# Optimization experiments

Hardware: AMD Instinct MI355X
Metric: run time of the kernel (lower is better)

Reference implementation:

```python
import jax, jax.numpy as jnp
import numpy as np

B, N, C, E, M = 16, 4096, 128, 12288, 64  # batch, nodes(seq_len), channels, incidences, hyperedges
NEG_SLOPE = 0.2
MARGIN = 4.2


def setup_inputs() -> dict:
    key = jax.random.key(0)
    k1, k2, k3, k4, k5 = jax.random.split(key, 5)
    x = jax.random.normal(k1, (B, N, C), jnp.float32)
    hyperedge_nodes = jax.random.randint(k2, (E,), 0, N)
    hyperedge_edges = jax.random.randint(k3, (E,), 0, M)
    weight = jax.random.normal(k4, (C, C), jnp.float32) * (1.0 / np.sqrt(C))  # glorot-ish
    att = jax.random.normal(k5, (1, 1, 2 * C), jnp.float32) * 0.1  # heads=1
    return {"x": x, "hyperedge_nodes": hyperedge_nodes, "hyperedge_edges": hyperedge_edges,
            "weight": weight, "att": att}


def _segment_softmax(logits, seg, num_segments):
    # logits: [E, B], softmax within groups of seg (per node)
    smax = jax.ops.segment_max(logits, seg, num_segments=num_segments)
    e = jnp.exp(logits - smax[seg])
    ssum = jax.ops.segment_sum(e, seg, num_segments=num_segments)
    return e / (ssum[seg] + 1e-16)


def reference(x, hyperedge_nodes, hyperedge_edges, weight, att):
    nodes = hyperedge_nodes
    edges = hyperedge_edges
    xw = jnp.matmul(x, weight)            # [B, N, C]
    x1 = jnp.swapaxes(xw, 0, 1)           # [N, B, C]

    x_gath = x1[nodes]                    # [E, B, C] gather by node id
    x_i = x_gath
    # per-hyperedge sum of incident node features (the python dict loop in torch)
    edge_sums = jax.ops.segment_sum(x_gath, edges, num_segments=M)  # [M, B, C]
    x_j = edge_sums[edges]                # [E, B, C]

    # O(M^2) pairwise hyperedge loss (vectorized)
    sq = jnp.sum(edge_sums * edge_sums, axis=-1)          # [M, B]
    norms = jnp.sqrt(sq)                                   # [M, B]
    inner = jnp.einsum('mbc,nbc->mnb', edge_sums, edge_sums)  # [M, M, B]
    cos = inner / (norms[:, None, :] * norms[None, :, :])      # [M, M, B]
    dist = jnp.sqrt(jnp.clip(sq[:, None, :] + sq[None, :, :] - 2.0 * inner, 0.0))
    loss_item = cos * dist + (1.0 - cos) * jnp.maximum(MARGIN - dist, 0.0)  # [M, M, B]
    loss_hyper = jnp.sum(jnp.abs(jnp.mean(loss_item, axis=-1))) / float((M + 1) ** 2)

    # attention per incidence, softmax grouped by node
    alpha = jnp.sum(jnp.concatenate([x_i, x_j], axis=-1) * att, axis=-1)  # [E, B]
    alpha = jax.nn.leaky_relu(alpha, NEG_SLOPE)
    alpha = _segment_softmax(alpha, nodes, N)  # [E, B] (dropout: eval mode, identity)

    ones = jnp.ones((E,), x.dtype)
    D = jax.ops.segment_sum(ones, nodes, num_segments=N)   # node degree
    Bdeg = jax.ops.segment_sum(ones, edges, num_segments=M)
    Bn = jnp.where(Bdeg > 0, 1.0 / Bdeg, 0.0)              # 1/deg, inf -> 0

    # propagate source_to_target: nodes -> hyperedges
    msg1 = Bn[edges][:, None, None] * x1[nodes] * alpha[:, :, None]   # [E, B, C]
    out_e = jax.ops.segment_sum(msg1, edges, num_segments=M)          # [M, B, C]
    # propagate target_to_source: hyperedges -> nodes
    msg2 = D[nodes][:, None, None] * out_e[edges] * alpha[:, :, None]
    out = jax.ops.segment_sum(msg2, nodes, num_segments=N)            # [N, B, C]
    out = jnp.swapaxes(out, 0, 1)                                     # [B, N, C]

    constrain_total = jnp.abs(jnp.mean(x_i - x_j)) + loss_hyper
    return (out, constrain_total)
```

## Files before the change

### kernel.cpp

```cpp
#include <hip/hip_runtime.h>
#include <hip/hip_bf16.h>

#define Bc 16
#define Nn 4096
#define Cc 128
#define Ee 12288
#define Mm 64
#define NEG_SLOPE 0.2f
#define MARGIN 4.2f
#define CH 4

__global__ __launch_bounds__(256) void gemm_xw(const float* __restrict__ x,
                                               const float* __restrict__ w,
                                               const float* __restrict__ att,
                                               float* __restrict__ xw,
                                               float* __restrict__ p,
                                               float* __restrict__ S1) {
    __shared__ float xT[64][132];
    __shared__ float wl[64][132];
    int t = threadIdx.x;
    int tc = t & 15;
    int tr = t >> 4;
    int rowbase = blockIdx.x * 128;

    float acc[8][8];
#pragma unroll
    for (int i = 0; i < 8; i++)
#pragma unroll
        for (int j = 0; j < 8; j++) acc[i][j] = 0.f;

    for (int half = 0; half < 2; ++half) {
#pragma unroll
        for (int s = 0; s < 8; ++s) {
            int idx = s * 256 + t;
            int row = idx >> 4, k4 = idx & 15;
            float4 v = ((const float4*)x)[(size_t)(rowbase + row) * 32 + half * 16 + k4];
            xT[k4 * 4 + 0][row] = v.x;
            xT[k4 * 4 + 1][row] = v.y;
            xT[k4 * 4 + 2][row] = v.z;
            xT[k4 * 4 + 3][row] = v.w;
        }
#pragma unroll
        for (int s = 0; s < 8; ++s) {
            int idx = s * 256 + t;
            int k = idx >> 5, c4 = idx & 31;
            float4 v = ((const float4*)w)[(size_t)(half * 64 + k) * 32 + c4];
            *(float4*)&wl[k][c4 * 4] = v;
        }
        __syncthreads();
#pragma unroll 4
        for (int k = 0; k < 64; ++k) {
            float4 xv0 = *(const float4*)&xT[k][tr * 8];
            float4 xv1 = *(const float4*)&xT[k][tr * 8 + 4];
            float4 wv0 = *(const float4*)&wl[k][tc * 8];
            float4 wv1 = *(const float4*)&wl[k][tc * 8 + 4];
            float xs_[8] = {xv0.x, xv0.y, xv0.z, xv0.w, xv1.x, xv1.y, xv1.z, xv1.w};
            float ww_[8] = {wv0.x, wv0.y, wv0.z, wv0.w, wv1.x, wv1.y, wv1.z, wv1.w};
#pragma unroll
            for (int i = 0; i < 8; i++)
#pragma unroll
                for (int j = 0; j < 8; j++) acc[i][j] += xs_[i] * ww_[j];
        }
        __syncthreads();
    }

    float4 a0 = ((const float4*)att)[tc * 2];
    float4 a1 = ((const float4*)att)[tc * 2 + 1];
    float aw[8] = {a0.x, a0.y, a0.z, a0.w, a1.x, a1.y, a1.z, a1.w};
#pragma unroll
    for (int i = 0; i < 8; i++) {
        int rr = rowbase + tr * 8 + i;
        int b = rr >> 12;
        int n = rr & 4095;
        ((float4*)xw)[(size_t)n * 512 + b * 32 + tc * 2] =
            make_float4(acc[i][0], acc[i][1], acc[i][2], acc[i][3]);
        ((float4*)xw)[(size_t)n * 512 + b * 32 + tc * 2 + 1] =
            make_float4(acc[i][4], acc[i][5], acc[i][6], acc[i][7]);
        float pd = 0.f, ss = 0.f;
#pragma unroll
        for (int j = 0; j < 8; j++) { pd += acc[i][j] * aw[j]; ss += acc[i][j]; }
#pragma unroll
        for (int m = 1; m < 16; m <<= 1) {
            pd += __shfl_xor(pd, m, 64);
            ss += __shfl_xor(ss, m, 64);
        }
        if (tc == 0) {
            p[n * 16 + b] = pd;
            atomicAdd(&S1[n], ss);
        }
    }
}

__global__ void hist_kernel(const int* __restrict__ nodes, const int* __restrict__ edges,
                            int* __restrict__ deg_n, int* __restrict__ deg_m) {
    int e = blockIdx.x * 256 + threadIdx.x;
    if (e < Ee) {
        atomicAdd(&deg_n[nodes[e]], 1);
        atomicAdd(&deg_m[edges[e]], 1);
    }
}

__global__ __launch_bounds__(1024) void scan_kernel(const int* __restrict__ deg_n,
                                                    const int* __restrict__ deg_m,
                                                    int* __restrict__ off_n, int* __restrict__ off_m,
                                                    int* __restrict__ cur_n, int* __restrict__ cur_m) {
    __shared__ int s[1024];
    int t = threadIdx.x;
    int base = t * 4;
    int d0 = deg_n[base], d1 = deg_n[base + 1], d2 = deg_n[base + 2], d3 = deg_n[base + 3];
    int local = d0 + d1 + d2 + d3;
    s[t] = local;
    __syncthreads();
    for (int offs = 1; offs < 1024; offs <<= 1) {
        int v = (t >= offs) ? s[t - offs] : 0;
        __syncthreads();
        s[t] += v;
        __syncthreads();
    }
    int excl = s[t] - local;
    int o0 = excl, o1 = excl + d0, o2 = excl + d0 + d1, o3 = excl + d0 + d1 + d2;
    off_n[base] = o0; off_n[base + 1] = o1; off_n[base + 2] = o2; off_n[base + 3] = o3;
    cur_n[base] = o0; cur_n[base + 1] = o1; cur_n[base + 2] = o2; cur_n[base + 3] = o3;
    if (t == 1023) off_n[4096] = s[1023];
    if (t == 0) {
        int acc = 0;
        for (int m = 0; m < 64; m++) {
            off_m[m] = acc; cur_m[m] = acc; acc += deg_m[m];
        }
        off_m[64] = acc;
    }
}

__global__ void fill_kernel(const int* __restrict__ nodes, const int* __restrict__ edges,
                            int* __restrict__ cur_n, int* __restrict__ cur_m,
                            int* __restrict__ list_n, int* __restrict__ gedge_n,
                            int* __restrict__ list_m, int* __restrict__ gnode_m) {
    int e = blockIdx.x * 256 + threadIdx.x;
    if (e < Ee) {
        int n = nodes[e], m = edges[e];
        int pos = atomicAdd(&cur_n[n], 1);
        list_n[pos] = e;
        gedge_n[pos] = m;
        int pos2 = atomicAdd(&cur_m[m], 1);
        list_m[pos2] = e;
        gnode_m[pos2] = n;
    }
}

__global__ __launch_bounds__(256) void edge_sums_kernel(const float* __restrict__ xw,
                                                        const int* __restrict__ off_m,
                                                        const int* __restrict__ gnode_m,
                                                        float* __restrict__ es) {
    int m = blockIdx.x;
    int slot = blockIdx.y * 256 + threadIdx.x;
    int beg = off_m[m], end = off_m[m + 1];
    int len = end - beg;
    int cbeg = beg + (len * (int)blockIdx.z) / CH;
    int cend = beg + (len * ((int)blockIdx.z + 1)) / CH;
    float acc = 0.f;
    for (int i = cbeg; i < cend; i++) {
        int n = gnode_m[i];
        acc += xw[(size_t)n * 2048 + slot];
    }
    if (acc != 0.f || cend > cbeg) atomicAdd(&es[m * 2048 + slot], acc);
}

__global__ __launch_bounds__(256) void edge_stats_kernel(const float* __restrict__ es,
                                                         const float* __restrict__ att,
                                                         float* __restrict__ q,
                                                         float* __restrict__ sq,
                                                         float* __restrict__ T) {
    int m = blockIdx.x, t = threadIdx.x;
    int b = t >> 4, oc = (t & 15) * 8;
    const float* row = es + m * 2048 + b * 128 + oc;
    float qd = 0.f, sqd = 0.f, s = 0.f;
#pragma unroll
    for (int j = 0; j < 8; j++) {
        float v = row[j];
        qd += v * att[128 + oc + j];
        sqd += v * v;
        s += v;
    }
    for (int k = 1; k < 16; k <<= 1) {
        qd += __shfl_xor(qd, k, 64);
        sqd += __shfl_xor(sqd, k, 64);
        s += __shfl_xor(s, k, 64);
    }
    if ((t & 15) == 0) { q[m * 16 + b] = qd; sq[m * 16 + b] = sqd; }
    s += __shfl_xor(s, 16, 64);
    s += __shfl_xor(s, 32, 64);
    __shared__ float ws4[4];
    if ((t & 63) == 0) ws4[t >> 6] = s;
    __syncthreads();
    if (t == 0) T[m] = ws4[0] + ws4[1] + ws4[2] + ws4[3];
}

__global__ __launch_bounds__(256) void loss_kernel(const float* __restrict__ es,
                                                   const float* __restrict__ sq,
                                                   float* __restrict__ loss_part) {
    int m = blockIdx.x, t = threadIdx.x;
    __shared__ float esm[2048];
    for (int i = t; i < 2048; i += 256) esm[i] = es[m * 2048 + i];
    __syncthreads();
    int n = t >> 2, bq = t & 3;
    float part = 0.f;
#pragma unroll
    for (int u = 0; u < 4; u++) {
        int b = bq * 4 + u;
        float inner = 0.f;
        const float* er = es + n * 2048 + b * 128;
        const float* em = esm + b * 128;
        for (int c = 0; c < 128; c += 4) {
            float4 a = *(const float4*)(em + c);
            float4 o = *(const float4*)(er + c);
            inner += a.x * o.x + a.y * o.y + a.z * o.z + a.w * o.w;
        }
        float sm = sq[m * 16 + b], sn = sq[n * 16 + b];
        float cosv = inner / (sqrtf(sm) * sqrtf(sn));
        float d2 = sm + sn - 2.f * inner;
        float dist = sqrtf(fmaxf(d2, 0.f));
        part += cosv * dist + (1.f - cosv) * fmaxf(MARGIN - dist, 0.f);
    }
    part += __shfl_xor(part, 1, 64);
    part += __shfl_xor(part, 2, 64);
    float labs = fabsf(part * (1.f / 16.f));
    __shared__ float pl[64];
    if (bq == 0) pl[n] = labs;
    __syncthreads();
    if (t < 64) {
        float v = pl[t];
        for (int k = 1; k < 64; k <<= 1) v += __shfl_xor(v, k, 64);
        if (t == 0) loss_part[m] = v;
    }
}

__global__ __launch_bounds__(256) void alpha_kernel(const int* __restrict__ off_n,
                                                    const int* __restrict__ list_n,
                                                    const int* __restrict__ gedge_n,
                                                    const float* __restrict__ p,
                                                    const float* __restrict__ q,
                                                    float* __restrict__ alpha) {
    int idx = blockIdx.x * 256 + threadIdx.x;
    int b = idx & 15, n = idx >> 4;
    int beg = off_n[n], end = off_n[n + 1];
    if (beg == end) return;
    float pb = p[n * 16 + b];
    float lf = pb + q[gedge_n[beg] * 16 + b];
    lf = lf >= 0.f ? lf : NEG_SLOPE * lf;
    float ssum = 0.f;
    for (int i = beg; i < end; i++) {
        float l = pb + q[gedge_n[i] * 16 + b];
        l = l >= 0.f ? l : NEG_SLOPE * l;
        ssum += __expf(l - lf);
    }
    float inv = 1.f / ssum;
    for (int i = beg; i < end; i++) {
        int e = list_n[i];
        float l = pb + q[gedge_n[i] * 16 + b];
        l = l >= 0.f ? l : NEG_SLOPE * l;
        alpha[e * 16 + b] = __expf(l - lf) * inv;
    }
}

__global__ __launch_bounds__(256) void out_e_kernel(const float* __restrict__ xw,
                                                    const int* __restrict__ off_m,
                                                    const int* __restrict__ list_m,
                                                    const int* __restrict__ gnode_m,
                                                    const float* __restrict__ alpha,
                                                    float* __restrict__ oute) {
    int m = blockIdx.x;
    int slot = blockIdx.y * 256 + threadIdx.x;
    int b = slot >> 7;
    int beg = off_m[m], end = off_m[m + 1];
    int len = end - beg;
    int cbeg = beg + (len * (int)blockIdx.z) / CH;
    int cend = beg + (len * ((int)blockIdx.z + 1)) / CH;
    float acc = 0.f;
    for (int i = cbeg; i < cend; i++) {
        int n = gnode_m[i];
        int e = list_m[i];
        acc += alpha[e * 16 + b] * xw[(size_t)n * 2048 + slot];
    }
    if (cend > cbeg) atomicAdd(&oute[m * 2048 + slot], acc);
}

__global__ __launch_bounds__(256) void out_kernel(const float* __restrict__ oute,
                                                  const int* __restrict__ off_n,
                                                  const int* __restrict__ list_n,
                                                  const int* __restrict__ gedge_n,
                                                  const int* __restrict__ deg_m,
                                                  const float* __restrict__ alpha,
                                                  float* __restrict__ out) {
    int n = blockIdx.x, t = threadIdx.x;
    int beg = off_n[n], end = off_n[n + 1];
    float d = (float)(end - beg);
    float acc[8] = {0, 0, 0, 0, 0, 0, 0, 0};
    for (int i = beg; i < end; i++) {
        int e = list_n[i];
        int m = gedge_n[i];
        float bn = 1.f / (float)deg_m[m];
        const float* er = oute + m * 2048;
#pragma unroll
        for (int k = 0; k < 8; k++) {
            int slot = t + k * 256;
            int b = slot >> 7;
            acc[k] += alpha[e * 16 + b] * bn * er[slot];
        }
    }
#pragma unroll
    for (int k = 0; k < 8; k++) {
        int slot = t + k * 256;
        int b = slot >> 7, c = slot & 127;
        out[(size_t)b * 524288 + n * 128 + c] = d * acc[k];
    }
}

__global__ __launch_bounds__(256) void finalize_kernel(const int* __restrict__ deg_n,
                                                       const float* __restrict__ S1,
                                                       const int* __restrict__ deg_m,
                                                       const float* __restrict__ T,
                                                       const float* __restrict__ loss_part,
                                                       float* __restrict__ out_scalar) {
    int t = threadIdx.x;
    double a = 0.0;
    for (int n = t; n < 4096; n += 256) a += (double)deg_n[n] * (double)S1[n];
    double bsum = 0.0, l = 0.0;
    if (t < 64) {
        bsum = (double)deg_m[t] * (double)T[t];
        l = (double)loss_part[t];
    }
    __shared__ double sa[256], sb[256], sl[256];
    sa[t] = a; sb[t] = bsum; sl[t] = l;
    __syncthreads();
    for (int s = 128; s > 0; s >>= 1) {
        if (t < s) { sa[t] += sa[t + s]; sb[t] += sb[t + s]; sl[t] += sl[t + s]; }
        __syncthreads();
    }
    if (t == 0) {
        double mean = (sa[0] - sb[0]) / 25165824.0;
        out_scalar[0] = (float)(fabs(mean) + sl[0] / 4225.0);
    }
}

extern "C" void kernel_launch(void* const* d_in, const int* in_sizes, int n_in,
                              void* d_out, int out_size, void* d_ws, size_t ws_size,
                              hipStream_t stream) {
    const float* x = (const float*)d_in[0];
    const int* nodes = (const int*)d_in[1];
    const int* edges = (const int*)d_in[2];
    const float* w = (const float*)d_in[3];
    const float* att = (const float*)d_in[4];
    float* out = (float*)d_out;

    char* ws = (char*)d_ws;
    size_t o = 0;
    float* xw = (float*)(ws + o);        o += (size_t)Nn * Bc * Cc * 4;
    size_t zbase = o;
    float* es = (float*)(ws + o);        o += (size_t)Mm * Bc * Cc * 4;
    float* oute = (float*)(ws + o);      o += (size_t)Mm * Bc * Cc * 4;
    int* deg_n = (int*)(ws + o);         o += (size_t)Nn * 4;
    int* deg_m = (int*)(ws + o);         o += (size_t)Mm * 4;
    float* S1 = (float*)(ws + o);        o += (size_t)Nn * 4;
    size_t zlen = o - zbase;
    float* p = (float*)(ws + o);         o += (size_t)Nn * Bc * 4;
    float* q = (float*)(ws + o);         o += (size_t)Mm * Bc * 4;
    float* sq = (float*)(ws + o);        o += (size_t)Mm * Bc * 4;
    float* alpha = (float*)(ws + o);     o += (size_t)Ee * Bc * 4;
    float* T = (float*)(ws + o);         o += (size_t)Mm * 4;
    float* loss_part = (float*)(ws + o); o += (size_t)Mm * 4;
    int* off_n = (int*)(ws + o);         o += (size_t)(Nn + 1) * 4;
    int* off_m = (int*)(ws + o);         o += (size_t)(Mm + 1) * 4;
    int* cur_n = (int*)(ws + o);         o += (size_t)Nn * 4;
    int* cur_m = (int*)(ws + o);         o += (size_t)Mm * 4;
    int* list_n = (int*)(ws + o);        o += (size_t)Ee * 4;
    int* gedge_n = (int*)(ws + o);       o += (size_t)Ee * 4;
    int* list_m = (int*)(ws + o);        o += (size_t)Ee * 4;
    int* gnode_m = (int*)(ws + o);       o += (size_t)Ee * 4;

    hipMemsetAsync(ws + zbase, 0, zlen, stream);

    gemm_xw<<<512, 256, 0, stream>>>(x, w, att, xw, p, S1);
    hist_kernel<<<48, 256, 0, stream>>>(nodes, edges, deg_n, deg_m);
    scan_kernel<<<1, 1024, 0, stream>>>(deg_n, deg_m, off_n, off_m, cur_n, cur_m);
    fill_kernel<<<48, 256, 0, stream>>>(nodes, edges, cur_n, cur_m,
                                        list_n, gedge_n, list_m, gnode_m);
    edge_sums_kernel<<<dim3(Mm, 8, CH), 256, 0, stream>>>(xw, off_m, gnode_m, es);
    edge_stats_kernel<<<Mm, 256, 0, stream>>>(es, att, q, sq, T);
    loss_kernel<<<Mm, 256, 0, stream>>>(es, sq, loss_part);
    alpha_kernel<<<256, 256, 0, stream>>>(off_n, list_n, gedge_n, p, q, alpha);
    out_e_kernel<<<dim3(Mm, 8, CH), 256, 0, stream>>>(xw, off_m, list_m, gnode_m, alpha, oute);
    out_kernel<<<Nn, 256, 0, stream>>>(oute, off_n, list_n, gedge_n, deg_m, alpha, out);
    finalize_kernel<<<1, 256, 0, stream>>>(deg_n, S1, deg_m, T, loss_part, out + (size_t)Bc * Nn * Cc);
}
```

Baseline: 257.5 us.

## Compute XW GEMM with split-bf16 MFMA instead of FP32 FMA

Replaces the FP32 SIMT tiled GEMM with bf16 MFMA instructions. Weight and x are each split into high and low bf16 parts, and three MFMAs (hi*hi, hi*lo, lo*hi) approximate FP32 precision. A small pre-kernel splits and swizzles the weight into LDS-friendly layout, and the GEMM loads the whole weight into LDS once per block. This aims to cut the cost of the 65536x128x128 GEMM, at the price of an extra kernel launch, slightly lower precision than true FP32, and scalar (non-vectorized) xw stores.

```diff
diff --git a/kernel.cpp b/kernel.cpp
--- a/kernel.cpp
+++ b/kernel.cpp
@@ -10,83 +10,122 @@
 #define MARGIN 4.2f
 #define CH 4
 
+typedef __attribute__((ext_vector_type(8))) short bfrag;
+typedef __attribute__((ext_vector_type(4))) float f32x4;
+
+__device__ inline unsigned short f2bf_rne(float f) {
+    unsigned u = __float_as_uint(f);
+    unsigned r = u + 0x7FFFu + ((u >> 16) & 1u);
+    return (unsigned short)(r >> 16);
+}
+__device__ inline float bfbits2f(unsigned short h) {
+    return __uint_as_float(((unsigned)h) << 16);
+}
+
+__global__ __launch_bounds__(256) void wsplit_kernel(const float* __restrict__ w,
+                                                     unsigned short* __restrict__ wsplit) {
+    int idx = blockIdx.x * 256 + threadIdx.x;
+    int k = idx >> 7, c = idx & 127;
+    float v = w[k * 128 + c];
+    unsigned short h = f2bf_rne(v);
+    float r = v - bfbits2f(h);
+    unsigned short lo = f2bf_rne(r);
+    int byteoff = c * 256 + ((2 * k) ^ ((c & 7) << 4));
+    *(unsigned short*)((char*)wsplit + byteoff) = h;
+    *(unsigned short*)((char*)wsplit + 32768 + byteoff) = lo;
+}
+
 __global__ __launch_bounds__(256) void gemm_xw(const float* __restrict__ x,
-                                               const float* __restrict__ w,
+                                               const unsigned short* __restrict__ wsplit,
                                                const float* __restrict__ att,
                                                float* __restrict__ xw,
                                                float* __restrict__ p,
                                                float* __restrict__ S1) {
-    __shared__ float xT[64][132];
-    __shared__ float wl[64][132];
+    __shared__ unsigned short wlds[32768];
     int t = threadIdx.x;
-    int tc = t & 15;
-    int tr = t >> 4;
-    int rowbase = blockIdx.x * 128;
-
-    float acc[8][8];
-#pragma unroll
-    for (int i = 0; i < 8; i++)
-#pragma unroll
-        for (int j = 0; j < 8; j++) acc[i][j] = 0.f;
-
-    for (int half = 0; half < 2; ++half) {
-#pragma unroll
-        for (int s = 0; s < 8; ++s) {
-            int idx = s * 256 + t;
-            int row = idx >> 4, k4 = idx & 15;
-            float4 v = ((const float4*)x)[(size_t)(rowbase + row) * 32 + half * 16 + k4];
-            xT[k4 * 4 + 0][row] = v.x;
-            xT[k4 * 4 + 1][row] = v.y;
-            xT[k4 * 4 + 2][row] = v.z;
-            xT[k4 * 4 + 3][row] = v.w;
-        }
-#pragma unroll
-        for (int s = 0; s < 8; ++s) {
-            int idx = s * 256 + t;
-            int k = idx >> 5, c4 = idx & 31;
-            float4 v = ((const float4*)w)[(size_t)(half * 64 + k) * 32 + c4];
-            *(float4*)&wl[k][c4 * 4] = v;
-        }
-        __syncthreads();
-#pragma unroll 4
-        for (int k = 0; k < 64; ++k) {
-            float4 xv0 = *(const float4*)&xT[k][tr * 8];
-            float4 xv1 = *(const float4*)&xT[k][tr * 8 + 4];
-            float4 wv0 = *(const float4*)&wl[k][tc * 8];
-            float4 wv1 = *(const float4*)&wl[k][tc * 8 + 4];
-            float xs_[8] = {xv0.x, xv0.y, xv0.z, xv0.w, xv1.x, xv1.y, xv1.z, xv1.w};
-            float ww_[8] = {wv0.x, wv0.y, wv0.z, wv0.w, wv1.x, wv1.y, wv1.z, wv1.w};
-#pragma unroll
-            for (int i = 0; i < 8; i++)
-#pragma unroll
-                for (int j = 0; j < 8; j++) acc[i][j] += xs_[i] * ww_[j];
-        }
-        __syncthreads();
-    }
-
-    float4 a0 = ((const float4*)att)[tc * 2];
-    float4 a1 = ((const float4*)att)[tc * 2 + 1];
-    float aw[8] = {a0.x, a0.y, a0.z, a0.w, a1.x, a1.y, a1.z, a1.w};
-#pragma unroll
-    for (int i = 0; i < 8; i++) {
-        int rr = rowbase + tr * 8 + i;
-        int b = rr >> 12;
-        int n = rr & 4095;
-        ((float4*)xw)[(size_t)n * 512 + b * 32 + tc * 2] =
-            make_float4(acc[i][0], acc[i][1], acc[i][2], acc[i][3]);
-        ((float4*)xw)[(size_t)n * 512 + b * 32 + tc * 2 + 1] =
-            make_float4(acc[i][4], acc[i][5], acc[i][6], acc[i][7]);
-        float pd = 0.f, ss = 0.f;
-#pragma unroll
-        for (int j = 0; j < 8; j++) { pd += acc[i][j] * aw[j]; ss += acc[i][j]; }
-#pragma unroll
-        for (int m = 1; m < 16; m <<= 1) {
-            pd += __shfl_xor(pd, m, 64);
-            ss += __shfl_xor(ss, m, 64);
-        }
-        if (tc == 0) {
-            p[n * 16 + b] = pd;
-            atomicAdd(&S1[n], ss);
+    {
+        const float4* g4 = (const float4*)wsplit;
+        float4* l4 = (float4*)wlds;
+#pragma unroll
+        for (int i = 0; i < 16; ++i) l4[i * 256 + t] = g4[i * 256 + t];
+    }
+    __syncthreads();
+
+    int w = t >> 6;
+    int l = t & 63;
+    int lrow = l & 15;
+    int lk = l >> 4;
+    int rowbase = blockIdx.x * 128 + w * 32;
+
+    f32x4 acc[2][8];
+#pragma unroll
+    for (int ti = 0; ti < 2; ++ti)
+#pragma unroll
+        for (int tj = 0; tj < 8; ++tj) acc[ti][tj] = (f32x4){0.f, 0.f, 0.f, 0.f};
+
+    for (int ks = 0; ks < 4; ++ks) {
+        bfrag bh[8], bl[8];
+        int kbyte = (64 * ks + 16 * lk) ^ ((l & 7) << 4);
+#pragma unroll
+        for (int tj = 0; tj < 8; ++tj) {
+            const char* base = (const char*)wlds + (tj * 16 + lrow) * 256 + kbyte;
+            bh[tj] = *(const bfrag*)base;
+            bl[tj] = *(const bfrag*)(base + 32768);
+        }
+#pragma unroll
+        for (int ti = 0; ti < 2; ++ti) {
+            int row = rowbase + ti * 16 + lrow;
+            const float4* xp = (const float4*)(x + (size_t)row * 128 + ks * 32 + lk * 8);
+            float4 v0 = xp[0], v1 = xp[1];
+            float fa[8] = {v0.x, v0.y, v0.z, v0.w, v1.x, v1.y, v1.z, v1.w};
+            bfrag ah, al;
+#pragma unroll
+            for (int j = 0; j < 8; ++j) {
+                unsigned u = __float_as_uint(fa[j]);
+                unsigned hb = u & 0xFFFF0000u;
+                float r = fa[j] - __uint_as_float(hb);
+                unsigned ru = __float_as_uint(r);
+                unsigned r2 = ru + 0x7FFFu + ((ru >> 16) & 1u);
+                ah[j] = (short)(hb >> 16);
+                al[j] = (short)(r2 >> 16);
+            }
+#pragma unroll
+            for (int tj = 0; tj < 8; ++tj) {
+                acc[ti][tj] = __builtin_amdgcn_mfma_f32_16x16x32_bf16(ah, bh[tj], acc[ti][tj], 0, 0, 0);
+                acc[ti][tj] = __builtin_amdgcn_mfma_f32_16x16x32_bf16(ah, bl[tj], acc[ti][tj], 0, 0, 0);
+                acc[ti][tj] = __builtin_amdgcn_mfma_f32_16x16x32_bf16(al, bh[tj], acc[ti][tj], 0, 0, 0);
+            }
+        }
+    }
+
+    float aw_[8];
+#pragma unroll
+    for (int tj = 0; tj < 8; ++tj) aw_[tj] = att[tj * 16 + lrow];
+#pragma unroll
+    for (int ti = 0; ti < 2; ++ti) {
+#pragma unroll
+        for (int v = 0; v < 4; ++v) {
+            int rr = rowbase + ti * 16 + lk * 4 + v;
+            int b = rr >> 12;
+            int n = rr & 4095;
+            float* orow = xw + (size_t)n * 2048 + b * 128;
+            float pd = 0.f, ss = 0.f;
+#pragma unroll
+            for (int tj = 0; tj < 8; ++tj) {
+                float val = acc[ti][tj][v];
+                orow[tj * 16 + lrow] = val;
+                pd += val * aw_[tj];
+                ss += val;
+            }
+#pragma unroll
+            for (int m = 1; m < 16; m <<= 1) {
+                pd += __shfl_xor(pd, m, 64);
+                ss += __shfl_xor(ss, m, 64);
+            }
+            if (lrow == 0) {
+                p[n * 16 + b] = pd;
+                atomicAdd(&S1[n], ss);
+            }
         }
     }
 }
@@ -366,6 +405,7 @@
     float* q = (float*)(ws + o);         o += (size_t)Mm * Bc * 4;
     float* sq = (float*)(ws + o);        o += (size_t)Mm * Bc * 4;
     float* alpha = (float*)(ws + o);     o += (size_t)Ee * Bc * 4;
+    unsigned short* wsplit = (unsigned short*)(ws + o); o += 65536;
     float* T = (float*)(ws + o);         o += (size_t)Mm * 4;
     float* loss_part = (float*)(ws + o); o += (size_t)Mm * 4;
     int* off_n = (int*)(ws + o);         o += (size_t)(Nn + 1) * 4;
@@ -379,7 +419,8 @@
 
     hipMemsetAsync(ws + zbase, 0, zlen, stream);
 
-    gemm_xw<<<512, 256, 0, stream>>>(x, w, att, xw, p, S1);
+    wsplit_kernel<<<64, 256, 0, stream>>>(w, wsplit);
+    gemm_xw<<<512, 256, 0, stream>>>(x, wsplit, att, xw, p, S1);
     hist_kernel<<<48, 256, 0, stream>>>(nodes, edges, deg_n, deg_m);
     scan_kernel<<<1, 1024, 0, stream>>>(deg_n, deg_m, off_n, off_m, cur_n, cur_m);
     fill_kernel<<<48, 256, 0, stream>>>(nodes, edges, cur_n, cur_m,
```

Result: faster. 243.4 us (-5.5%).
